# Kernel tuning notes

Measured on AMD Instinct MI355X. Metric: run time of the kernel, lower is better.

Reference implementation:

```python
import jax, jax.numpy as jnp
import numpy as np

B, FNP, D = 16, 4096, 512
P, S, F = 16, 8, 32

def setup_inputs() -> dict:
    key = jax.random.key(0)
    k1, k2 = jax.random.split(key)
    token_states = jax.random.normal(k1, (B, FNP, D), dtype=jnp.float32)
    W = jax.random.normal(k2, (2 * P, D), dtype=jnp.float32) * 0.02
    b = jnp.zeros((2 * P,), dtype=jnp.float32)
    return {"token_states": token_states, "W": W, "b": b, "T": 1032}

def reference(token_states, W, b, T):
    Bsz, FNp, Dm = token_states.shape
    Np = FNp // F
    h = token_states.reshape(Bsz, F, Np, Dm)
    # per-patch linear head: [B, F, Np, 2P]
    raw = jnp.einsum('bfnd,ed->bfne', h, W) + b
    raw = raw.reshape(Bsz, F, Np, 2, P)
    mu = raw[:, :, :, 0, :]                                   # [B, F, Np, P]
    sigma = jnp.clip(jnp.exp(raw[:, :, :, 1, :]), 1e-06, None)
    mu = jnp.transpose(mu, (0, 2, 3, 1))                      # [B, Np, P, F]
    sigma = jnp.transpose(sigma, (0, 2, 3, 1))
    # overlap-add fold: time index for each (patch, offset)
    t = (jnp.arange(Np)[:, None] * S + jnp.arange(P)[None, :]).reshape(-1)  # [Np*P]
    valid = (t < T)
    t_c = jnp.where(valid, t, 0)
    vmask = valid.astype(mu.dtype)[None, :, None]             # [1, Np*P, 1]
    mu_flat = mu.reshape(Bsz, Np * P, F) * vmask
    sg_flat = sigma.reshape(Bsz, Np * P, F) * vmask
    mu_full = jnp.zeros((Bsz, T, F), dtype=mu.dtype).at[:, t_c, :].add(mu_flat)
    sigma_full = jnp.zeros((Bsz, T, F), dtype=mu.dtype).at[:, t_c, :].add(sg_flat)
    counts = jnp.zeros((T,), dtype=mu.dtype).at[t_c].add(valid.astype(mu.dtype))
    counts = jnp.clip(counts, 1.0, None)[None, :, None]       # [1, T, 1]
    return (mu_full / counts, sigma_full / counts)
```

## Files before the change

### kernel.cpp

```cpp
#include <hip/hip_runtime.h>
#include <math.h>

#define B_   16
#define F_   32
#define NP_  128
#define D_   512
#define P_   16
#define KC   32
#define NCH  (D_ / KC)
#define BUFW (NP_ * KC)

typedef __attribute__((ext_vector_type(8)))  short  short8;
typedef __attribute__((ext_vector_type(16))) float  floatx16;

union Frag { short8 v; unsigned int u[4]; };

__device__ inline unsigned int cvt_pk_bf16(float lo, float hi) {
    unsigned int r;
    asm volatile("v_cvt_pk_bf16_f32 %0, %1, %2" : "=v"(r) : "v"(lo), "v"(hi));
    return r;
}

__global__ __launch_bounds__(512, 4)
void pd_kernel(const float* __restrict__ ts,
               const float* __restrict__ W,
               const float* __restrict__ bias,
               float* __restrict__ out, int T)
{
    __shared__ float smem[4 * BUFW];

    const int tid  = threadIdx.x;
    const int lane = tid & 63;
    const int wave = tid >> 6;
    const int mt   = wave & 3;
    const int p    = wave >> 2;

    const int d = blockIdx.x;
    const int b = (d & 7) | ((d >> 8) << 3);
    const int f = (d >> 3) & 31;
    const float* __restrict__ tsb = ts + ((size_t)b * F_ + f) * NP_ * D_;

    auto STAGE = [&](int cc) {
        const int k0 = cc * KC;
        float* dstb = smem + (cc & 3) * BUFW;
#pragma unroll
        for (int it = 0; it < 2; ++it) {
            int slot = it * 512 + tid;
            int rr = slot >> 3;
            int ql = slot & 7;
            int qg = ql ^ (rr & 7);
            const float* src = tsb + rr * D_ + k0 + (qg << 2);
            __builtin_amdgcn_global_load_lds(
                (const __attribute__((address_space(1))) unsigned int*)src,
                (__attribute__((address_space(3))) unsigned int*)&dstb[slot << 2],
                16, 0, 0);
        }
    };

    const int e_b = lane & 31;
    const int kh  = lane >> 5;
    Frag bf[NCH];
    {
        const float* wb = W + (size_t)e_b * D_ + kh * 8;
#pragma unroll
        for (int c = 0; c < NCH; ++c) {
            const int k = c * 32 + p * 16;
            const float4 lo = *(const float4*)(wb + k);
            const float4 hi = *(const float4*)(wb + k + 4);
            bf[c].u[0] = cvt_pk_bf16(lo.x, lo.y);
            bf[c].u[1] = cvt_pk_bf16(lo.z, lo.w);
            bf[c].u[2] = cvt_pk_bf16(hi.x, hi.y);
            bf[c].u[3] = cvt_pk_bf16(hi.z, hi.w);
        }
    }
    __builtin_amdgcn_sched_barrier(0);
    STAGE(0);
    STAGE(1);
    __builtin_amdgcn_sched_barrier(0);

    floatx16 acc;
#pragma unroll
    for (int r = 0; r < 16; ++r) acc[r] = 0.f;

    const int rl     = lane & 31;
    const int ldsrow = mt * 32 + rl;
    const int sw8    = ldsrow & 7;
    const int q0     = p * 4 + kh * 2;

#pragma unroll
    for (int c = 0; c < NCH; ++c) {
        if (c + 2 < NCH) {
            STAGE(c + 2);
            asm volatile("s_waitcnt vmcnt(4)\n\ts_barrier" ::: "memory");
        } else if (c == NCH - 2) {
            asm volatile("s_waitcnt vmcnt(2)\n\ts_barrier" ::: "memory");
        } else {
            asm volatile("s_waitcnt vmcnt(0)\n\ts_barrier" ::: "memory");
        }
        __builtin_amdgcn_sched_barrier(0);

        const float4* rowp = (const float4*)(smem + (c & 3) * BUFW + ldsrow * KC);
        const float4 lo = rowp[q0 ^ sw8];
        const float4 hi = rowp[(q0 + 1) ^ sw8];
        Frag a;
        a.u[0] = cvt_pk_bf16(lo.x, lo.y);
        a.u[1] = cvt_pk_bf16(lo.z, lo.w);
        a.u[2] = cvt_pk_bf16(hi.x, hi.y);
        a.u[3] = cvt_pk_bf16(hi.z, hi.w);
        acc = __builtin_amdgcn_mfma_f32_32x32x16_bf16(a.v, bf[c].v, acc, 0, 0, 0);
    }

    if (p == 0) {
#pragma unroll
        for (int r = 0; r < 16; ++r) {
            const int rowl = (r & 3) + 8 * (r >> 2) + 4 * kh;
            smem[(mt * 32 + rowl) * 33 + e_b] = acc[r];
        }
    }
    __syncthreads();
    if (p == 1) {
#pragma unroll
        for (int r = 0; r < 16; ++r) {
            const int rowl = (r & 3) + 8 * (r >> 2) + 4 * kh;
            smem[(mt * 32 + rowl) * 33 + e_b] += acc[r];
        }
    }
    __syncthreads();

#pragma unroll
    for (int jj = 0; jj < 8; ++jj) {
        const int item = tid * 8 + jj;
        const int n = item >> 5;
        const int e = item & 31;
        float v = smem[n * 33 + e] + bias[e];
        if (e >= P_) v = fmaxf(expf(v), 1e-6f);
        smem[n * 33 + e] = v;
    }
    __syncthreads();

    const int TF = T * F_;
    const size_t halfoff = (size_t)B_ * TF;
    for (int item = tid; item < 2 * T; item += 512) {
        const int half = (item >= T) ? 1 : 0;
        const int t    = item - half * T;
        const int nmax = min(NP_ - 1, t >> 3);
        const int nmin = (t > 8) ? ((t - 8) >> 3) : 0;
        float sum = 0.f;
        const int cnt = nmax - nmin + 1;
        for (int nn = nmin; nn <= nmax; ++nn)
            sum += smem[nn * 33 + (half << 4) + (t - (nn << 3))];
        const float r = (cnt > 0) ? sum / (float)cnt : 0.f;
        out[(size_t)half * halfoff + (size_t)b * TF + (size_t)t * F_ + f] = r;
    }
}

extern "C" void kernel_launch(void* const* d_in, const int* in_sizes, int n_in,
                              void* d_out, int out_size, void* d_ws, size_t ws_size,
                              hipStream_t stream)
{
    const float* ts   = (const float*)d_in[0];
    const float* W    = (const float*)d_in[1];
    const float* bias = (const float*)d_in[2];
    float* out = (float*)d_out;

    const int T = out_size / (2 * B_ * F_);

    dim3 grid(B_ * F_);
    dim3 block(512);
    pd_kernel<<<grid, block, 0, stream>>>(ts, W, bias, out, T);
}
```

Before: 42.88 us.

## Load MFMA operands directly from global into registers with 4-deep prefetch

Replaces the LDS-staged, barrier-synchronized pipeline for token states with direct per-lane float4 global loads into registers, prefetched four K-steps ahead and gated by vmcnt waits. W fragments are also streamed per step instead of preloaded into registers. This removes the LDS round trip and the per-chunk block barriers and shrinks shared memory to the epilogue buffer, which may allow more blocks per CU. In exchange, each lane reads 32-byte row segments with a stride of 512 floats, so global coalescing is worse and W is re-read from cache at every step.

```diff
diff --git a/kernel.cpp b/kernel.cpp
--- a/kernel.cpp
+++ b/kernel.cpp
@@ -6,9 +6,7 @@
 #define NP_  128
 #define D_   512
 #define P_   16
-#define KC   32
-#define NCH  (D_ / KC)
-#define BUFW (NP_ * KC)
+#define NS   16
 
 typedef __attribute__((ext_vector_type(8)))  short  short8;
 typedef __attribute__((ext_vector_type(16))) float  floatx16;
@@ -27,7 +25,7 @@
                const float* __restrict__ bias,
                float* __restrict__ out, int T)
 {
-    __shared__ float smem[4 * BUFW];
+    __shared__ float smem[NP_ * 33];
 
     const int tid  = threadIdx.x;
     const int lane = tid & 63;
@@ -40,74 +38,56 @@
     const int f = (d >> 3) & 31;
     const float* __restrict__ tsb = ts + ((size_t)b * F_ + f) * NP_ * D_;
 
-    auto STAGE = [&](int cc) {
-        const int k0 = cc * KC;
-        float* dstb = smem + (cc & 3) * BUFW;
+    const int e_b  = lane & 31;
+    const int kh   = lane >> 5;
+    const int arow = mt * 32 + e_b;
+    const float* __restrict__ aptr = tsb + (size_t)arow * D_ + kh * 8;
+    const float* __restrict__ bptr = W + (size_t)e_b * D_ + kh * 8;
+
+    float4 alo[4], ahi[4], blo[4], bhi[4];
 #pragma unroll
-        for (int it = 0; it < 2; ++it) {
-            int slot = it * 512 + tid;
-            int rr = slot >> 3;
-            int ql = slot & 7;
-            int qg = ql ^ (rr & 7);
-            const float* src = tsb + rr * D_ + k0 + (qg << 2);
-            __builtin_amdgcn_global_load_lds(
-                (const __attribute__((address_space(1))) unsigned int*)src,
-                (__attribute__((address_space(3))) unsigned int*)&dstb[slot << 2],
-                16, 0, 0);
-        }
-    };
-
-    const int e_b = lane & 31;
-    const int kh  = lane >> 5;
-    Frag bf[NCH];
-    {
-        const float* wb = W + (size_t)e_b * D_ + kh * 8;
-#pragma unroll
-        for (int c = 0; c < NCH; ++c) {
-            const int k = c * 32 + p * 16;
-            const float4 lo = *(const float4*)(wb + k);
-            const float4 hi = *(const float4*)(wb + k + 4);
-            bf[c].u[0] = cvt_pk_bf16(lo.x, lo.y);
-            bf[c].u[1] = cvt_pk_bf16(lo.z, lo.w);
-            bf[c].u[2] = cvt_pk_bf16(hi.x, hi.y);
-            bf[c].u[3] = cvt_pk_bf16(hi.z, hi.w);
-        }
+    for (int t = 0; t < 4; ++t) {
+        const int off = (2 * t + p) * 16;
+        alo[t] = *(const float4*)(aptr + off);
+        ahi[t] = *(const float4*)(aptr + off + 4);
+        blo[t] = *(const float4*)(bptr + off);
+        bhi[t] = *(const float4*)(bptr + off + 4);
     }
-    __builtin_amdgcn_sched_barrier(0);
-    STAGE(0);
-    STAGE(1);
     __builtin_amdgcn_sched_barrier(0);
 
     floatx16 acc;
 #pragma unroll
     for (int r = 0; r < 16; ++r) acc[r] = 0.f;
 
-    const int rl     = lane & 31;
-    const int ldsrow = mt * 32 + rl;
-    const int sw8    = ldsrow & 7;
-    const int q0     = p * 4 + kh * 2;
+#pragma unroll
+    for (int t = 0; t < NS; ++t) {
+        if (t <= 12)      asm volatile("s_waitcnt vmcnt(12)" ::: "memory");
+        else if (t == 13) asm volatile("s_waitcnt vmcnt(8)"  ::: "memory");
+        else if (t == 14) asm volatile("s_waitcnt vmcnt(4)"  ::: "memory");
+        else              asm volatile("s_waitcnt vmcnt(0)"  ::: "memory");
+        __builtin_amdgcn_sched_barrier(0);
 
-#pragma unroll
-    for (int c = 0; c < NCH; ++c) {
-        if (c + 2 < NCH) {
-            STAGE(c + 2);
-            asm volatile("s_waitcnt vmcnt(4)\n\ts_barrier" ::: "memory");
-        } else if (c == NCH - 2) {
-            asm volatile("s_waitcnt vmcnt(2)\n\ts_barrier" ::: "memory");
-        } else {
-            asm volatile("s_waitcnt vmcnt(0)\n\ts_barrier" ::: "memory");
+        const int sl = t & 3;
+        Frag a, bb;
+        a.u[0]  = cvt_pk_bf16(alo[sl].x, alo[sl].y);
+        a.u[1]  = cvt_pk_bf16(alo[sl].z, alo[sl].w);
+        a.u[2]  = cvt_pk_bf16(ahi[sl].x, ahi[sl].y);
+        a.u[3]  = cvt_pk_bf16(ahi[sl].z, ahi[sl].w);
+        bb.u[0] = cvt_pk_bf16(blo[sl].x, blo[sl].y);
+        bb.u[1] = cvt_pk_bf16(blo[sl].z, blo[sl].w);
+        bb.u[2] = cvt_pk_bf16(bhi[sl].x, bhi[sl].y);
+        bb.u[3] = cvt_pk_bf16(bhi[sl].z, bhi[sl].w);
+
+        if (t + 4 < NS) {
+            const int off = (2 * (t + 4) + p) * 16;
+            alo[sl] = *(const float4*)(aptr + off);
+            ahi[sl] = *(const float4*)(aptr + off + 4);
+            blo[sl] = *(const float4*)(bptr + off);
+            bhi[sl] = *(const float4*)(bptr + off + 4);
         }
         __builtin_amdgcn_sched_barrier(0);
 
-        const float4* rowp = (const float4*)(smem + (c & 3) * BUFW + ldsrow * KC);
-        const float4 lo = rowp[q0 ^ sw8];
-        const float4 hi = rowp[(q0 + 1) ^ sw8];
-        Frag a;
-        a.u[0] = cvt_pk_bf16(lo.x, lo.y);
-        a.u[1] = cvt_pk_bf16(lo.z, lo.w);
-        a.u[2] = cvt_pk_bf16(hi.x, hi.y);
-        a.u[3] = cvt_pk_bf16(hi.z, hi.w);
-        acc = __builtin_amdgcn_mfma_f32_32x32x16_bf16(a.v, bf[c].v, acc, 0, 0, 0);
+        acc = __builtin_amdgcn_mfma_f32_32x32x16_bf16(a.v, bb.v, acc, 0, 0, 0);
     }
 
     if (p == 0) {
```

New measurement: 47.24 us. 1.1x slower.

## Process two feature slices per block with deeper 8-stage LDS prefetch ring

Applied to the files above, without the earlier changes.

Each block now handles two f-slices, halving the grid to 256 blocks. The LDS ring grows from 4 to 8 stages with 7 chunks in flight, and it prefetches the second slice's chunks while the first slice's epilogue runs. This hides the epilogue and prologue latency and amortizes the W fragment load across two slices. In exchange, LDS use rises to about 145KB per block, so occupancy drops to one block per CU, and the grid of 256 blocks matches the CU count with no tail balancing.

```diff
diff --git a/kernel.cpp b/kernel.cpp
--- a/kernel.cpp
+++ b/kernel.cpp
@@ -1,14 +1,16 @@
 #include <hip/hip_runtime.h>
 #include <math.h>
 
-#define B_   16
-#define F_   32
-#define NP_  128
-#define D_   512
-#define P_   16
-#define KC   32
-#define NCH  (D_ / KC)
-#define BUFW (NP_ * KC)
+#define B_    16
+#define F_    32
+#define NP_   128
+#define D_    512
+#define P_    16
+#define KC    32
+#define NCH   16
+#define BUFW  (NP_ * KC)
+#define NRING 8
+#define EOFF  (NRING * BUFW)
 
 typedef __attribute__((ext_vector_type(8)))  short  short8;
 typedef __attribute__((ext_vector_type(16))) float  floatx16;
@@ -21,13 +23,15 @@
     return r;
 }
 
+#define EBAR asm volatile("s_waitcnt lgkmcnt(0)\n\ts_barrier" ::: "memory")
+
 __global__ __launch_bounds__(512, 4)
 void pd_kernel(const float* __restrict__ ts,
                const float* __restrict__ W,
                const float* __restrict__ bias,
                float* __restrict__ out, int T)
 {
-    __shared__ float smem[4 * BUFW];
+    __shared__ float smem[EOFF + NP_ * 33];
 
     const int tid  = threadIdx.x;
     const int lane = tid & 63;
@@ -35,24 +39,23 @@
     const int mt   = wave & 3;
     const int p    = wave >> 2;
 
-    const int d = blockIdx.x;
-    const int b = (d & 7) | ((d >> 8) << 3);
-    const int f = (d >> 3) & 31;
-    const float* __restrict__ tsb = ts + ((size_t)b * F_ + f) * NP_ * D_;
+    const int d  = blockIdx.x;
+    const int b  = (d & 7) | (((d >> 7) & 1) << 3);
+    const int fp = (d >> 3) & 15;
+    const float* __restrict__ tsb0 = ts + ((size_t)(b * F_ + 2 * fp) * NP_) * D_;
+    const float* __restrict__ tsb1 = tsb0 + (size_t)NP_ * D_;
 
-    auto STAGE = [&](int cc) {
-        const int k0 = cc * KC;
-        float* dstb = smem + (cc & 3) * BUFW;
+    auto STAGE = [&](const float* base, int cc) {
 #pragma unroll
         for (int it = 0; it < 2; ++it) {
-            int slot = it * 512 + tid;
-            int rr = slot >> 3;
-            int ql = slot & 7;
-            int qg = ql ^ (rr & 7);
-            const float* src = tsb + rr * D_ + k0 + (qg << 2);
+            const int slot = it * 512 + tid;
+            const int r2 = slot >> 3;
+            const int qg = (slot & 7) ^ (r2 & 7);
+            const float* src = base + r2 * D_ + cc * KC + (qg << 2);
+            float* dst = smem + (cc & 7) * BUFW + (slot << 2);
             __builtin_amdgcn_global_load_lds(
                 (const __attribute__((address_space(1))) unsigned int*)src,
-                (__attribute__((address_space(3))) unsigned int*)&dstb[slot << 2],
+                (__attribute__((address_space(3))) unsigned int*)dst,
                 16, 0, 0);
         }
     };
@@ -74,83 +77,105 @@
         }
     }
     __builtin_amdgcn_sched_barrier(0);
-    STAGE(0);
-    STAGE(1);
+
+#pragma unroll
+    for (int c = 0; c < 7; ++c) STAGE(tsb0, c);
     __builtin_amdgcn_sched_barrier(0);
 
-    floatx16 acc;
-#pragma unroll
-    for (int r = 0; r < 16; ++r) acc[r] = 0.f;
-
-    const int rl     = lane & 31;
-    const int ldsrow = mt * 32 + rl;
+    const int ldsrow = mt * 32 + (lane & 31);
     const int sw8    = ldsrow & 7;
-    const int q0     = p * 4 + kh * 2;
-
-#pragma unroll
-    for (int c = 0; c < NCH; ++c) {
-        if (c + 2 < NCH) {
-            STAGE(c + 2);
-            asm volatile("s_waitcnt vmcnt(4)\n\ts_barrier" ::: "memory");
-        } else if (c == NCH - 2) {
-            asm volatile("s_waitcnt vmcnt(2)\n\ts_barrier" ::: "memory");
-        } else {
-            asm volatile("s_waitcnt vmcnt(0)\n\ts_barrier" ::: "memory");
-        }
-        __builtin_amdgcn_sched_barrier(0);
-
-        const float4* rowp = (const float4*)(smem + (c & 3) * BUFW + ldsrow * KC);
-        const float4 lo = rowp[q0 ^ sw8];
-        const float4 hi = rowp[(q0 + 1) ^ sw8];
-        Frag a;
-        a.u[0] = cvt_pk_bf16(lo.x, lo.y);
-        a.u[1] = cvt_pk_bf16(lo.z, lo.w);
-        a.u[2] = cvt_pk_bf16(hi.x, hi.y);
-        a.u[3] = cvt_pk_bf16(hi.z, hi.w);
-        acc = __builtin_amdgcn_mfma_f32_32x32x16_bf16(a.v, bf[c].v, acc, 0, 0, 0);
-    }
-
-    if (p == 0) {
-#pragma unroll
-        for (int r = 0; r < 16; ++r) {
-            const int rowl = (r & 3) + 8 * (r >> 2) + 4 * kh;
-            smem[(mt * 32 + rowl) * 33 + e_b] = acc[r];
-        }
-    }
-    __syncthreads();
-    if (p == 1) {
-#pragma unroll
-        for (int r = 0; r < 16; ++r) {
-            const int rowl = (r & 3) + 8 * (r >> 2) + 4 * kh;
-            smem[(mt * 32 + rowl) * 33 + e_b] += acc[r];
-        }
-    }
-    __syncthreads();
-
-#pragma unroll
-    for (int jj = 0; jj < 8; ++jj) {
-        const int item = tid * 8 + jj;
-        const int n = item >> 5;
-        const int e = item & 31;
-        float v = smem[n * 33 + e] + bias[e];
-        if (e >= P_) v = fmaxf(expf(v), 1e-6f);
-        smem[n * 33 + e] = v;
-    }
-    __syncthreads();
+    const int aq     = p * 4 + kh * 2;
 
     const int TF = T * F_;
     const size_t halfoff = (size_t)B_ * TF;
-    for (int item = tid; item < 2 * T; item += 512) {
-        const int half = (item >= T) ? 1 : 0;
-        const int t    = item - half * T;
-        const int nmax = min(NP_ - 1, t >> 3);
-        const int nmin = (t > 8) ? ((t - 8) >> 3) : 0;
-        float sum = 0.f;
-        const int cnt = nmax - nmin + 1;
-        for (int nn = nmin; nn <= nmax; ++nn)
-            sum += smem[nn * 33 + (half << 4) + (t - (nn << 3))];
-        const float r = (cnt > 0) ? sum / (float)cnt : 0.f;
-        out[(size_t)half * halfoff + (size_t)b * TF + (size_t)t * F_ + f] = r;
+    float* const E = smem + EOFF;
+
+#pragma unroll
+    for (int q = 0; q < 2; ++q) {
+        const float* __restrict__ tscur = q ? tsb1 : tsb0;
+
+        floatx16 acc;
+#pragma unroll
+        for (int r = 0; r < 16; ++r) acc[r] = 0.f;
+
+#pragma unroll
+        for (int c = 0; c < NCH; ++c) {
+            if (q == 0 || c <= 9)
+                asm volatile("s_waitcnt vmcnt(12)\n\ts_barrier" ::: "memory");
+            else if (c == 10)
+                asm volatile("s_waitcnt vmcnt(10)\n\ts_barrier" ::: "memory");
+            else if (c == 11)
+                asm volatile("s_waitcnt vmcnt(8)\n\ts_barrier" ::: "memory");
+            else if (c == 12)
+                asm volatile("s_waitcnt vmcnt(6)\n\ts_barrier" ::: "memory");
+            else if (c == 13)
+                asm volatile("s_waitcnt vmcnt(4)\n\ts_barrier" ::: "memory");
+            else if (c == 14)
+                asm volatile("s_waitcnt vmcnt(2)\n\ts_barrier" ::: "memory");
+            else
+                asm volatile("s_waitcnt vmcnt(0)\n\ts_barrier" ::: "memory");
+            __builtin_amdgcn_sched_barrier(0);
+
+            if (q == 0) {
+                if (c <= 8) STAGE(tsb0, c + 7);
+                else        STAGE(tsb1, c - 9);
+            } else {
+                if (c <= 8) STAGE(tsb1, c + 7);
+            }
+            __builtin_amdgcn_sched_barrier(0);
+
+            const float* rowp = smem + (c & 7) * BUFW + ldsrow * KC;
+            const float4 lo = *(const float4*)(rowp + ((aq ^ sw8) << 2));
+            const float4 hi = *(const float4*)(rowp + (((aq + 1) ^ sw8) << 2));
+            Frag a;
+            a.u[0] = cvt_pk_bf16(lo.x, lo.y);
+            a.u[1] = cvt_pk_bf16(lo.z, lo.w);
+            a.u[2] = cvt_pk_bf16(hi.x, hi.y);
+            a.u[3] = cvt_pk_bf16(hi.z, hi.w);
+            acc = __builtin_amdgcn_mfma_f32_32x32x16_bf16(a.v, bf[c].v, acc, 0, 0, 0);
+        }
+
+        const int f = 2 * fp + q;
+        if (p == 0) {
+#pragma unroll
+            for (int r = 0; r < 16; ++r) {
+                const int rowl = (r & 3) + 8 * (r >> 2) + 4 * kh;
+                E[(mt * 32 + rowl) * 33 + e_b] = acc[r];
+            }
+        }
+        EBAR;
+        if (p == 1) {
+#pragma unroll
+            for (int r = 0; r < 16; ++r) {
+                const int rowl = (r & 3) + 8 * (r >> 2) + 4 * kh;
+                E[(mt * 32 + rowl) * 33 + e_b] += acc[r];
+            }
+        }
+        EBAR;
+
+#pragma unroll
+        for (int jj = 0; jj < 8; ++jj) {
+            const int item = tid * 8 + jj;
+            const int n = item >> 5;
+            const int e = item & 31;
+            float v = E[n * 33 + e] + bias[e];
+            if (e >= P_) v = fmaxf(expf(v), 1e-6f);
+            E[n * 33 + e] = v;
+        }
+        EBAR;
+
+        for (int item = tid; item < 2 * T; item += 512) {
+            const int half = (item >= T) ? 1 : 0;
+            const int t    = item - half * T;
+            const int nmax = min(NP_ - 1, t >> 3);
+            const int nmin = (t > 8) ? ((t - 8) >> 3) : 0;
+            float sum = 0.f;
+            const int cnt = nmax - nmin + 1;
+            for (int nn = nmin; nn <= nmax; ++nn)
+                sum += E[nn * 33 + (half << 4) + (t - (nn << 3))];
+            const float r = (cnt > 0) ? sum / (float)cnt : 0.f;
+            out[(size_t)half * halfoff + (size_t)b * TF + (size_t)t * F_ + f] = r;
+        }
     }
 }
 
@@ -165,7 +190,7 @@
 
     const int T = out_size / (2 * B_ * F_);
 
-    dim3 grid(B_ * F_);
+    dim3 grid(B_ * F_ / 2);
     dim3 block(512);
     pd_kernel<<<grid, block, 0, stream>>>(ts, W, bias, out, T);
 }
```

Result: faster. 39.54 us (-7.8%).
